# Kernel tuning notes

Hardware: AMD Instinct MI355X
Metric: run time of the kernel (lower is better)

Reference implementation:

```python
import jax, jax.numpy as jnp
import numpy as np

SQRT2 = 1.4142135623730951
B, C, T, J = 32, 4, 262144, 8


def _dw_corr(x, f):
    # depthwise VALID cross-correlation of (B,C,T) with 1-D filter f
    ch = x.shape[1]
    w = jnp.tile(f[None, None, :], (ch, 1, 1))  # (C,1,m)
    return jax.lax.conv_general_dilated(
        x, w, (1,), 'VALID', feature_group_count=ch,
        dimension_numbers=('NCH', 'OIH', 'NCH'))


def colfilter(x, h):
    # 'same' true convolution with odd-length filter h, zero padding
    p = h.shape[0] // 2
    xp = jnp.pad(x, ((0, 0), (0, 0), (p, p)))
    return _dw_corr(xp, jnp.flip(h))


def colifilt(x, ha, hb):
    # dtcwt synthesis upsampling filter bank (even-length qshift filters,
    # m//2 odd for 10-tap), zero extension (padding_mode='zeros').
    # Output length 2T; phase convention of dtcwt colifilt with ta=t, tb=t-1.
    b, c, t = x.shape
    m2 = ha.shape[0] // 2  # 5 for 10-tap qshift
    xp = jnp.pad(x, ((0, 0), (0, 0), (m2, m2)))  # length t+10
    L = t // 2 + 4
    seq_b = xp[:, :, 1::2][:, :, :L]      # padded indices 1,3,...,t+7
    seq_a = xp[:, :, 0::2][:, :, 1:L + 1]  # padded indices 2,4,...,t+8
    hao, hae = jnp.flip(ha[0::2]), jnp.flip(ha[1::2])  # odd/even taps of tree-a filter
    hbo, hbe = jnp.flip(hb[0::2]), jnp.flip(hb[1::2])
    y0 = _dw_corr(seq_b, hao)  # output samples 4s
    y1 = _dw_corr(seq_a, hbo)  # 4s+1
    y2 = _dw_corr(seq_b, hae)  # 4s+2
    y3 = _dw_corr(seq_a, hbe)  # 4s+3
    return jnp.stack([y0, y1, y2, y3], axis=-1).reshape(b, c, 2 * t)


def c2q(bp_r, bp_i, scale):
    # complex -> real: real part to even samples, imag part to odd samples
    b, c, th = bp_r.shape
    return (jnp.stack([bp_r, bp_i], axis=-1) * scale).reshape(b, c, 2 * th)


def inv_j2plus(lo, bp_r, bp_i, g0a, g1a, g0b, g1b):
    # one coarse synthesis level: interleave complex bandpass, then
    hi = c2q(bp_r, bp_i, SQRT2)
    return colifilt(lo, g0b, g0a) + colifilt(hi, g1b, g1a)


def inv_j1(lo, bp_r, bp_i, g0o, g1o):
    # finest synthesis level: full-rate biorthogonal filters, no upsampling
    hi = c2q(bp_r, bp_i, SQRT2)
    return colfilter(lo, g0o) + colfilter(hi, g1o)


def setup_inputs():
    key = jax.random.key(0)
    ks = jax.random.split(key, 32)
    inp = {}
    inp['yl'] = jax.random.normal(ks[0], (B, C, T // 2 ** (J - 1)), jnp.float32)
    for j in range(J):
        tj = T // 2 ** (j + 1)
        inp[f'yh{j}_r'] = jax.random.normal(ks[2 * j + 1], (B, C, tj), jnp.float32)
        inp[f'yh{j}_i'] = jax.random.normal(ks[2 * j + 2], (B, C, tj), jnp.float32)

    def filt(k, n):
        f = jax.random.normal(k, (n,), jnp.float32)
        return f / jnp.linalg.norm(f)

    inp['g0o'] = filt(ks[20], 7)   # near_sym_a synthesis lowpass (7-tap)
    inp['g1o'] = filt(ks[21], 5)   # near_sym_a synthesis highpass (5-tap)
    g0a = filt(ks[22], 10)         # qshift_a 10-tap
    g1a = filt(ks[23], 10)
    inp['g0a'], inp['g0b'] = g0a, jnp.flip(g0a)  # tree-b = time-reversed tree-a
    inp['g1a'], inp['g1b'] = g1a, jnp.flip(g1a)
    return inp


def reference(yl, yh0_r, yh0_i, yh1_r, yh1_i, yh2_r, yh2_i, yh3_r, yh3_i,
              yh4_r, yh4_i, yh5_r, yh5_i, yh6_r, yh6_i, yh7_r, yh7_i,
              g0o, g1o, g0a, g0b, g1a, g1b):
    yh = [(yh0_r, yh0_i), (yh1_r, yh1_i), (yh2_r, yh2_i), (yh3_r, yh3_i),
          (yh4_r, yh4_i), (yh5_r, yh5_i), (yh6_r, yh6_i), (yh7_r, yh7_i)]
    x = yl
    for j in range(J - 1, 0, -1):  # coarse-to-fine, doubles length each level
        x = inv_j2plus(x, yh[j][0], yh[j][1], g0a, g1a, g0b, g1b)
    return inv_j1(x, yh[0][0], yh[0][1], g0o, g1o)
```

## Files before the change

### kernel.cpp

```cpp
#include <hip/hip_runtime.h>

#define BLOCK 256
#define FT 1024

static __device__ __forceinline__ float ldz(const float* __restrict__ p, int i, int n) {
    return (i >= 0 && i < n) ? p[i] : 0.f;
}

struct QFilt {
    float b0e[5], b0o[5], a0e[5], a0o[5];
    float b1e[5], b1o[5], a1e[5], a1o[5];
};

static __device__ __forceinline__ QFilt load_qfilt(
    const float* __restrict__ g0a, const float* __restrict__ g0b,
    const float* __restrict__ g1a, const float* __restrict__ g1b) {
    const float S2 = 1.4142135623730951f;
    QFilt f;
#pragma unroll
    for (int i = 0; i < 5; ++i) {
        f.b0e[i] = g0b[8 - 2 * i]; f.b0o[i] = g0b[9 - 2 * i];
        f.a0e[i] = g0a[8 - 2 * i]; f.a0o[i] = g0a[9 - 2 * i];
        f.b1e[i] = S2 * g1b[8 - 2 * i]; f.b1o[i] = S2 * g1b[9 - 2 * i];
        f.a1e[i] = S2 * g1a[8 - 2 * i]; f.a1o[i] = S2 * g1a[9 - 2 * i];
    }
    return f;
}

static __device__ __forceinline__ float4 quad_i(
    const float* __restrict__ lo_s, int lobase,
    const float* __restrict__ r_s, const float* __restrict__ i_s, int ribase,
    const QFilt& f) {
    float y0 = 0.f, y1 = 0.f, y2 = 0.f, y3 = 0.f;
#pragma unroll
    for (int i = 0; i < 5; ++i) {
        float ve = lo_s[lobase + 2 * i], vo = lo_s[lobase + 2 * i + 1];
        float vr = r_s[ribase + i], vi = i_s[ribase + i];
        y0 = fmaf(ve, f.b0e[i], y0); y2 = fmaf(ve, f.b0o[i], y2);
        y1 = fmaf(vo, f.a0e[i], y1); y3 = fmaf(vo, f.a0o[i], y3);
        y0 = fmaf(vr, f.b1e[i], y0); y2 = fmaf(vr, f.b1o[i], y2);
        y1 = fmaf(vi, f.a1e[i], y1); y3 = fmaf(vi, f.a1o[i], y3);
    }
    return make_float4(y0, y1, y2, y3);
}

static __device__ __forceinline__ float4 quad_d(
    const float* __restrict__ Ae, const float* __restrict__ Ao, int base,
    const float* __restrict__ r_s, const float* __restrict__ i_s, int ribase,
    const QFilt& f) {
    float y0 = 0.f, y1 = 0.f, y2 = 0.f, y3 = 0.f;
#pragma unroll
    for (int i = 0; i < 5; ++i) {
        float ve = Ae[base + i], vo = Ao[base + i];
        float vr = r_s[ribase + i], vi = i_s[ribase + i];
        y0 = fmaf(ve, f.b0e[i], y0); y2 = fmaf(ve, f.b0o[i], y2);
        y1 = fmaf(vo, f.a0e[i], y1); y3 = fmaf(vo, f.a0o[i], y3);
        y0 = fmaf(vr, f.b1e[i], y0); y2 = fmaf(vr, f.b1o[i], y2);
        y1 = fmaf(vi, f.a1e[i], y1); y3 = fmaf(vi, f.a1o[i], y3);
    }
    return make_float4(y0, y1, y2, y3);
}

__global__ void __launch_bounds__(BLOCK) pair_lvl(
    const float* __restrict__ up,
    const float* __restrict__ ru, const float* __restrict__ iu,
    const float* __restrict__ rl, const float* __restrict__ il,
    float* __restrict__ out,
    const float* __restrict__ g0a, const float* __restrict__ g0b,
    const float* __restrict__ g1a, const float* __restrict__ g1b,
    int L)
{
    __shared__ __align__(16) float upw[272], ruw[140], iuw[140], rlw[264], ilw[264];
    __shared__ __align__(16) float Ae[260], Ao[260];
    int tid = threadIdx.x, bx = blockIdx.x, row = blockIdx.y;
    int lup = L >> 2, lu8 = L >> 3, lql = L >> 2;
    const float* uprow = up + (size_t)row * lup;
    const float* rurow = ru + (size_t)row * lu8;
    const float* iurow = iu + (size_t)row * lu8;
    const float* rlrow = rl + (size_t)row * lql;
    const float* ilrow = il + (size_t)row * lql;
    bool bnd = (bx == 0) || (bx == (int)gridDim.x - 1);
    int S = bx << 8;
    int sAu = (S >> 1) - 1;
    int gu = S - 8;
    int gru = (S >> 1) - 4;
    int grl = S - 4;

    for (int i = tid; i < 270; i += BLOCK) {
        const float* src; float* dst; int k, gb, len;
        if (i < 68)       { src = uprow; dst = upw; k = i;       gb = gu + 4 * k;  len = lup; }
        else if (i < 103) { src = rurow; dst = ruw; k = i - 68;  gb = gru + 4 * k; len = lu8; }
        else if (i < 138) { src = iurow; dst = iuw; k = i - 103; gb = gru + 4 * k; len = lu8; }
        else if (i < 204) { src = rlrow; dst = rlw; k = i - 138; gb = grl + 4 * k; len = lql; }
        else              { src = ilrow; dst = ilw; k = i - 204; gb = grl + 4 * k; len = lql; }
        float4 v;
        if (!bnd) v = *reinterpret_cast<const float4*>(src + gb);
        else { v.x = ldz(src, gb, len); v.y = ldz(src, gb + 1, len);
               v.z = ldz(src, gb + 2, len); v.w = ldz(src, gb + 3, len); }
        *reinterpret_cast<float4*>(dst + 4 * k) = v;
    }
    __syncthreads();

    QFilt f = load_qfilt(g0a, g0b, g1a, g1b);
    if (tid < 130) {
        float4 q = quad_i(upw, 2 * tid + 2, ruw, iuw, tid + 1, f);
        if (bnd) {
            int sp = sAu + tid;
            if (sp < 0 || sp >= lu8) q = make_float4(0.f, 0.f, 0.f, 0.f);
        }
        Ae[2 * tid] = q.x; Ae[2 * tid + 1] = q.z;
        Ao[2 * tid] = q.y; Ao[2 * tid + 1] = q.w;
    }
    __syncthreads();

    float4 res = quad_d(Ae, Ao, tid, rlw, ilw, tid + 2, f);
    reinterpret_cast<float4*>(out + (size_t)row * L)[S + tid] = res;
}

__global__ void __launch_bounds__(BLOCK) final4_lvl(
    const float* __restrict__ x4,
    const float* __restrict__ r3, const float* __restrict__ i3,
    const float* __restrict__ r2, const float* __restrict__ i2,
    const float* __restrict__ r1, const float* __restrict__ i1,
    const float* __restrict__ r0, const float* __restrict__ i0,
    float* __restrict__ out,
    const float* __restrict__ g0a, const float* __restrict__ g0b,
    const float* __restrict__ g1a, const float* __restrict__ g1b,
    const float* __restrict__ g0o, const float* __restrict__ g1o,
    int T_)
{
    const float S2 = 1.4142135623730951f;
    __shared__ __align__(16) float x4w[152], r3w[80], i3w[80];
    __shared__ __align__(16) float r2w[144], i2w[144];
    __shared__ __align__(16) float r1w[264], i1w[264];
    __shared__ __align__(16) float x3s[280], x2s[528];
    __shared__ __align__(16) float4 x1q[258];

    int row = blockIdx.y, tid = threadIdx.x;
    int n0 = blockIdx.x * FT;
    int t2 = T_ >> 1, t4 = T_ >> 2, t8 = T_ >> 3, t16 = T_ >> 4;
    int s0 = n0 >> 2, u0 = n0 >> 3, v0 = n0 >> 4, h0 = n0 >> 1;
    const float* x4row = x4 + (size_t)row * t8;
    const float* r3row = r3 + (size_t)row * t16;
    const float* i3row = i3 + (size_t)row * t16;
    const float* r2row = r2 + (size_t)row * t8;
    const float* i2row = i2 + (size_t)row * t8;
    const float* r1row = r1 + (size_t)row * t4;
    const float* i1row = i1 + (size_t)row * t4;
    const float* r0row = r0 + (size_t)row * t2;
    const float* i0row = i0 + (size_t)row * t2;
    bool bnd = (blockIdx.x == 0) || ((int)blockIdx.x == (int)gridDim.x - 1);

    float rA[4], iA[4];
    {
        int u0e = h0 + 2 * tid - 1;
        if (!bnd) {
            float4 va = *reinterpret_cast<const float4*>(r0row + u0e);
            float4 vb = *reinterpret_cast<const float4*>(i0row + u0e);
            rA[0] = va.x; rA[1] = va.y; rA[2] = va.z; rA[3] = va.w;
            iA[0] = vb.x; iA[1] = vb.y; iA[2] = vb.z; iA[3] = vb.w;
        } else {
#pragma unroll
            for (int e = 0; e < 4; ++e) {
                rA[e] = ldz(r0row, u0e + e, t2);
                iA[e] = ldz(i0row, u0e + e, t2);
            }
        }
    }
    float g0r[7], g1r[5];
#pragma unroll
    for (int j = 0; j < 7; ++j) g0r[j] = g0o[j];
#pragma unroll
    for (int j = 0; j < 5; ++j) g1r[j] = S2 * g1o[j];

    for (int i = tid; i < 277; i += BLOCK) {
        const float* src; float* dst; int k, gb, len;
        if (i < 37)       { src = x4row; dst = x4w; k = i;       gb = 2 * v0 - 8 + 4 * k; len = t8; }
        else if (i < 56)  { src = r3row; dst = r3w; k = i - 37;  gb = v0 - 4 + 4 * k;     len = t16; }
        else if (i < 75)  { src = i3row; dst = i3w; k = i - 56;  gb = v0 - 4 + 4 * k;     len = t16; }
        else if (i < 110) { src = r2row; dst = r2w; k = i - 75;  gb = u0 - 4 + 4 * k;     len = t8; }
        else if (i < 145) { src = i2row; dst = i2w; k = i - 110; gb = u0 - 4 + 4 * k;     len = t8; }
        else if (i < 211) { src = r1row; dst = r1w; k = i - 145; gb = s0 - 4 + 4 * k;     len = t4; }
        else              { src = i1row; dst = i1w; k = i - 211; gb = s0 - 4 + 4 * k;     len = t4; }
        float4 v;
        if (!bnd) v = *reinterpret_cast<const float4*>(src + gb);
        else { v.x = ldz(src, gb, len); v.y = ldz(src, gb + 1, len);
               v.z = ldz(src, gb + 2, len); v.w = ldz(src, gb + 3, len); }
        *reinterpret_cast<float4*>(dst + 4 * k) = v;
    }
    __syncthreads();

    QFilt f = load_qfilt(g0a, g0b, g1a, g1b);

    if (tid < 69) {
        int k = tid;
        float4 q = quad_i(x4w, 2 * k, r3w, i3w, k, f);
        if (bnd) {
            int v = v0 - 2 + k;
            if (v < 0 || v >= t16) q = make_float4(0.f, 0.f, 0.f, 0.f);
        }
        reinterpret_cast<float4*>(x3s)[k] = q;
    }
    __syncthreads();

    if (tid < 132) {
        int k = tid;
        float4 q = quad_i(x3s, 2 * k, r2w, i2w, k, f);
        if (bnd) {
            int u = u0 - 2 + k;
            if (u < 0 || u >= t8) q = make_float4(0.f, 0.f, 0.f, 0.f);
        }
        reinterpret_cast<float4*>(x2s)[k] = q;
    }
    __syncthreads();

    float4 myq;
    {
        int l = tid;
        float4 q = quad_i(x2s, 2 * l + 2, r1w, i1w, l + 1, f);
        if (bnd) {
            int s = s0 - 1 + l;
            if (s < 0 || s >= t4) q = make_float4(0.f, 0.f, 0.f, 0.f);
        }
        myq = q;
        x1q[l] = q;
        if (tid < 2) {
            int l2 = 256 + tid;
            q = quad_i(x2s, 2 * l2 + 2, r1w, i1w, l2 + 1, f);
            if (bnd) {
                int s = s0 - 1 + l2;
                if (s < 0 || s >= t4) q = make_float4(0.f, 0.f, 0.f, 0.f);
            }
            x1q[l2] = q;
        }
    }
    __syncthreads();

    float w[12];
    *reinterpret_cast<float4*>(&w[0]) = myq;
    *reinterpret_cast<float4*>(&w[4]) = x1q[tid + 1];
    *reinterpret_cast<float4*>(&w[8]) = x1q[tid + 2];

    float o[4];
#pragma unroll
    for (int p = 0; p < 4; ++p) {
        float acc = 0.f;
#pragma unroll
        for (int j = 0; j < 7; ++j)
            acc = fmaf(g0r[j], w[p + 7 - j], acc);
#pragma unroll
        for (int j = 0; j < 5; ++j) {
            int e = p + 4 - j;
            float v = (e & 1) ? iA[e >> 1] : rA[e >> 1];
            acc = fmaf(g1r[j], v, acc);
        }
        o[p] = acc;
    }
    reinterpret_cast<float4*>(out + (size_t)row * T_)[s0 + tid] =
        make_float4(o[0], o[1], o[2], o[3]);
}

extern "C" void kernel_launch(void* const* d_in, const int* in_sizes, int n_in,
                              void* d_out, int out_size, void* d_ws, size_t ws_size,
                              hipStream_t stream)
{
    const float* yl = (const float*)d_in[0];
    const float* yhr[8]; const float* yhi[8];
    for (int j = 0; j < 8; ++j) {
        yhr[j] = (const float*)d_in[1 + 2 * j];
        yhi[j] = (const float*)d_in[2 + 2 * j];
    }
    const float* g0o = (const float*)d_in[17];
    const float* g1o = (const float*)d_in[18];
    const float* g0a = (const float*)d_in[19];
    const float* g0b = (const float*)d_in[20];
    const float* g1a = (const float*)d_in[21];
    const float* g1b = (const float*)d_in[22];

    const int BC = 32 * 4;
    const int T_ = 262144;

    float* x4buf = (float*)d_ws;
    float* x6buf = (float*)((char*)d_ws + ((size_t)32 << 20));

    {
        dim3 grid(8192 / 1024, BC);
        pair_lvl<<<grid, BLOCK, 0, stream>>>(
            yl, yhr[7], yhi[7], yhr[6], yhi[6], x6buf,
            g0a, g0b, g1a, g1b, 8192);
    }
    {
        dim3 grid(32768 / 1024, BC);
        pair_lvl<<<grid, BLOCK, 0, stream>>>(
            x6buf, yhr[5], yhi[5], yhr[4], yhi[4], x4buf,
            g0a, g0b, g1a, g1b, 32768);
    }
    dim3 grid(T_ / FT, BC);
    final4_lvl<<<grid, BLOCK, 0, stream>>>(
        x4buf, yhr[3], yhi[3], yhr[2], yhi[2], yhr[1], yhi[1],
        yhr[0], yhi[0], (float*)d_out,
        g0a, g0b, g1a, g1b, g0o, g1o, T_);
}
```

Baseline: 127.6 us.

## Make final four-level kernel persistent with register-prefetched next-tile loads

Converts the final synthesis kernel into a persistent grid of 32 blocks per row. Each block loops over tiles with a stride and prefetches the next tile's inputs into registers while it computes the current one, overlapping global loads with the LDS filter stages. It also swaps __syncthreads for an explicit lgkmcnt wait plus s_barrier, so barriers do not wait on outstanding global prefetches. Filter loads and setup are hoisted out of the tile loop. The cost is a much smaller grid (4096 blocks instead of 32768), which may leave the GPU with less parallelism to hide latency, and more live registers from the prefetch buffers.

Measured after the change: 144.2 us. +13.0%, slower.

```diff
diff --git a/kernel.cpp b/kernel.cpp
--- a/kernel.cpp
+++ b/kernel.cpp
@@ -2,6 +2,12 @@
 
 #define BLOCK 256
 #define FT 1024
+#define PSTRIDE 32
+
+#define BAR_LGKM() do { \
+    asm volatile("s_waitcnt lgkmcnt(0)" ::: "memory"); \
+    __builtin_amdgcn_s_barrier(); \
+} while (0)
 
 static __device__ __forceinline__ float ldz(const float* __restrict__ p, int i, int n) {
     return (i >= 0 && i < n) ? p[i] : 0.f;
@@ -117,7 +123,7 @@
     reinterpret_cast<float4*>(out + (size_t)row * L)[S + tid] = res;
 }
 
-__global__ void __launch_bounds__(BLOCK) final4_lvl(
+__global__ void __launch_bounds__(BLOCK) final4_persist(
     const float* __restrict__ x4,
     const float* __restrict__ r3, const float* __restrict__ i3,
     const float* __restrict__ r2, const float* __restrict__ i2,
@@ -137,9 +143,8 @@
     __shared__ __align__(16) float4 x1q[258];
 
     int row = blockIdx.y, tid = threadIdx.x;
-    int n0 = blockIdx.x * FT;
     int t2 = T_ >> 1, t4 = T_ >> 2, t8 = T_ >> 3, t16 = T_ >> 4;
-    int s0 = n0 >> 2, u0 = n0 >> 3, v0 = n0 >> 4, h0 = n0 >> 1;
+    int NT = T_ >> 10;
     const float* x4row = x4 + (size_t)row * t8;
     const float* r3row = r3 + (size_t)row * t16;
     const float* i3row = i3 + (size_t)row * t16;
@@ -149,115 +154,167 @@
     const float* i1row = i1 + (size_t)row * t4;
     const float* r0row = r0 + (size_t)row * t2;
     const float* i0row = i0 + (size_t)row * t2;
-    bool bnd = (blockIdx.x == 0) || ((int)blockIdx.x == (int)gridDim.x - 1);
-
-    float rA[4], iA[4];
-    {
-        int u0e = h0 + 2 * tid - 1;
-        if (!bnd) {
-            float4 va = *reinterpret_cast<const float4*>(r0row + u0e);
-            float4 vb = *reinterpret_cast<const float4*>(i0row + u0e);
-            rA[0] = va.x; rA[1] = va.y; rA[2] = va.z; rA[3] = va.w;
-            iA[0] = vb.x; iA[1] = vb.y; iA[2] = vb.z; iA[3] = vb.w;
+
+    const float* src0; float* dst0; int A0, C0, len0;
+    {
+        int i = tid, k;
+        if (i < 37)       { src0 = x4row; k = i;       dst0 = x4w + 4 * k; A0 = 128; C0 = -8 + 4 * k; len0 = t8; }
+        else if (i < 56)  { src0 = r3row; k = i - 37;  dst0 = r3w + 4 * k; A0 = 64;  C0 = -4 + 4 * k; len0 = t16; }
+        else if (i < 75)  { src0 = i3row; k = i - 56;  dst0 = i3w + 4 * k; A0 = 64;  C0 = -4 + 4 * k; len0 = t16; }
+        else if (i < 110) { src0 = r2row; k = i - 75;  dst0 = r2w + 4 * k; A0 = 128; C0 = -4 + 4 * k; len0 = t8; }
+        else if (i < 145) { src0 = i2row; k = i - 110; dst0 = i2w + 4 * k; A0 = 128; C0 = -4 + 4 * k; len0 = t8; }
+        else if (i < 211) { src0 = r1row; k = i - 145; dst0 = r1w + 4 * k; A0 = 256; C0 = -4 + 4 * k; len0 = t4; }
+        else              { src0 = i1row; k = i - 211; dst0 = i1w + 4 * k; A0 = 256; C0 = -4 + 4 * k; len0 = t4; }
+    }
+    bool has1 = (tid < 21);
+    int k1 = tid + 45;
+    float* dst1 = i1w + 4 * k1;
+    int C1 = -4 + 4 * k1;
+
+    QFilt f = load_qfilt(g0a, g0b, g1a, g1b);
+    float g0r[7], g1r[5];
+#pragma unroll
+    for (int j = 0; j < 7; ++j) g0r[j] = g0o[j];
+#pragma unroll
+    for (int j = 0; j < 5; ++j) g1r[j] = S2 * g1o[j];
+
+    int tile = blockIdx.x;
+    bool bndc = (tile == 0) || (tile == NT - 1);
+    float4 pv0, pv1 = make_float4(0.f, 0.f, 0.f, 0.f);
+    {
+        int gb = A0 * tile + C0;
+        if (!bndc) pv0 = *reinterpret_cast<const float4*>(src0 + gb);
+        else { pv0.x = ldz(src0, gb, len0); pv0.y = ldz(src0, gb + 1, len0);
+               pv0.z = ldz(src0, gb + 2, len0); pv0.w = ldz(src0, gb + 3, len0); }
+        if (has1) {
+            int gb1 = 256 * tile + C1;
+            if (!bndc) pv1 = *reinterpret_cast<const float4*>(i1row + gb1);
+            else { pv1.x = ldz(i1row, gb1, t4); pv1.y = ldz(i1row, gb1 + 1, t4);
+                   pv1.z = ldz(i1row, gb1 + 2, t4); pv1.w = ldz(i1row, gb1 + 3, t4); }
+        }
+    }
+    float4 prA_c, piA_c, prA_n = make_float4(0,0,0,0), piA_n = make_float4(0,0,0,0);
+    {
+        int u0e = (tile << 9) + 2 * tid - 1;
+        if (!bndc) {
+            prA_c = *reinterpret_cast<const float4*>(r0row + u0e);
+            piA_c = *reinterpret_cast<const float4*>(i0row + u0e);
         } else {
-#pragma unroll
-            for (int e = 0; e < 4; ++e) {
-                rA[e] = ldz(r0row, u0e + e, t2);
-                iA[e] = ldz(i0row, u0e + e, t2);
-            }
-        }
-    }
-    float g0r[7], g1r[5];
-#pragma unroll
-    for (int j = 0; j < 7; ++j) g0r[j] = g0o[j];
-#pragma unroll
-    for (int j = 0; j < 5; ++j) g1r[j] = S2 * g1o[j];
-
-    for (int i = tid; i < 277; i += BLOCK) {
-        const float* src; float* dst; int k, gb, len;
-        if (i < 37)       { src = x4row; dst = x4w; k = i;       gb = 2 * v0 - 8 + 4 * k; len = t8; }
-        else if (i < 56)  { src = r3row; dst = r3w; k = i - 37;  gb = v0 - 4 + 4 * k;     len = t16; }
-        else if (i < 75)  { src = i3row; dst = i3w; k = i - 56;  gb = v0 - 4 + 4 * k;     len = t16; }
-        else if (i < 110) { src = r2row; dst = r2w; k = i - 75;  gb = u0 - 4 + 4 * k;     len = t8; }
-        else if (i < 145) { src = i2row; dst = i2w; k = i - 110; gb = u0 - 4 + 4 * k;     len = t8; }
-        else if (i < 211) { src = r1row; dst = r1w; k = i - 145; gb = s0 - 4 + 4 * k;     len = t4; }
-        else              { src = i1row; dst = i1w; k = i - 211; gb = s0 - 4 + 4 * k;     len = t4; }
-        float4 v;
-        if (!bnd) v = *reinterpret_cast<const float4*>(src + gb);
-        else { v.x = ldz(src, gb, len); v.y = ldz(src, gb + 1, len);
-               v.z = ldz(src, gb + 2, len); v.w = ldz(src, gb + 3, len); }
-        *reinterpret_cast<float4*>(dst + 4 * k) = v;
-    }
-    __syncthreads();
-
-    QFilt f = load_qfilt(g0a, g0b, g1a, g1b);
-
-    if (tid < 69) {
-        int k = tid;
-        float4 q = quad_i(x4w, 2 * k, r3w, i3w, k, f);
-        if (bnd) {
-            int v = v0 - 2 + k;
-            if (v < 0 || v >= t16) q = make_float4(0.f, 0.f, 0.f, 0.f);
-        }
-        reinterpret_cast<float4*>(x3s)[k] = q;
-    }
-    __syncthreads();
-
-    if (tid < 132) {
-        int k = tid;
-        float4 q = quad_i(x3s, 2 * k, r2w, i2w, k, f);
-        if (bnd) {
-            int u = u0 - 2 + k;
-            if (u < 0 || u >= t8) q = make_float4(0.f, 0.f, 0.f, 0.f);
-        }
-        reinterpret_cast<float4*>(x2s)[k] = q;
-    }
-    __syncthreads();
-
-    float4 myq;
-    {
-        int l = tid;
-        float4 q = quad_i(x2s, 2 * l + 2, r1w, i1w, l + 1, f);
-        if (bnd) {
-            int s = s0 - 1 + l;
-            if (s < 0 || s >= t4) q = make_float4(0.f, 0.f, 0.f, 0.f);
-        }
-        myq = q;
-        x1q[l] = q;
-        if (tid < 2) {
-            int l2 = 256 + tid;
-            q = quad_i(x2s, 2 * l2 + 2, r1w, i1w, l2 + 1, f);
-            if (bnd) {
-                int s = s0 - 1 + l2;
+            prA_c.x = ldz(r0row, u0e, t2);     prA_c.y = ldz(r0row, u0e + 1, t2);
+            prA_c.z = ldz(r0row, u0e + 2, t2); prA_c.w = ldz(r0row, u0e + 3, t2);
+            piA_c.x = ldz(i0row, u0e, t2);     piA_c.y = ldz(i0row, u0e + 1, t2);
+            piA_c.z = ldz(i0row, u0e + 2, t2); piA_c.w = ldz(i0row, u0e + 3, t2);
+        }
+    }
+
+    bool bndn = false;
+    while (true) {
+        *reinterpret_cast<float4*>(dst0) = pv0;
+        if (has1) *reinterpret_cast<float4*>(dst1) = pv1;
+        BAR_LGKM();
+
+        int ntile = tile + PSTRIDE;
+        bool nvalid = ntile < NT;
+        if (nvalid) {
+            bndn = (ntile == NT - 1);
+            int gb = A0 * ntile + C0;
+            if (!bndn) pv0 = *reinterpret_cast<const float4*>(src0 + gb);
+            else { pv0.x = ldz(src0, gb, len0); pv0.y = ldz(src0, gb + 1, len0);
+                   pv0.z = ldz(src0, gb + 2, len0); pv0.w = ldz(src0, gb + 3, len0); }
+            if (has1) {
+                int gb1 = 256 * ntile + C1;
+                if (!bndn) pv1 = *reinterpret_cast<const float4*>(i1row + gb1);
+                else { pv1.x = ldz(i1row, gb1, t4); pv1.y = ldz(i1row, gb1 + 1, t4);
+                       pv1.z = ldz(i1row, gb1 + 2, t4); pv1.w = ldz(i1row, gb1 + 3, t4); }
+            }
+            int u0e = (ntile << 9) + 2 * tid - 1;
+            if (!bndn) {
+                prA_n = *reinterpret_cast<const float4*>(r0row + u0e);
+                piA_n = *reinterpret_cast<const float4*>(i0row + u0e);
+            } else {
+                prA_n.x = ldz(r0row, u0e, t2);     prA_n.y = ldz(r0row, u0e + 1, t2);
+                prA_n.z = ldz(r0row, u0e + 2, t2); prA_n.w = ldz(r0row, u0e + 3, t2);
+                piA_n.x = ldz(i0row, u0e, t2);     piA_n.y = ldz(i0row, u0e + 1, t2);
+                piA_n.z = ldz(i0row, u0e + 2, t2); piA_n.w = ldz(i0row, u0e + 3, t2);
+            }
+        }
+
+        int s0 = tile << 8, u0 = tile << 7, v0 = tile << 6;
+
+        if (tid < 69) {
+            int k = tid;
+            float4 q = quad_i(x4w, 2 * k, r3w, i3w, k, f);
+            if (bndc) {
+                int v = v0 - 2 + k;
+                if (v < 0 || v >= t16) q = make_float4(0.f, 0.f, 0.f, 0.f);
+            }
+            reinterpret_cast<float4*>(x3s)[k] = q;
+        }
+        BAR_LGKM();
+
+        if (tid < 132) {
+            int k = tid;
+            float4 q = quad_i(x3s, 2 * k, r2w, i2w, k, f);
+            if (bndc) {
+                int u = u0 - 2 + k;
+                if (u < 0 || u >= t8) q = make_float4(0.f, 0.f, 0.f, 0.f);
+            }
+            reinterpret_cast<float4*>(x2s)[k] = q;
+        }
+        BAR_LGKM();
+
+        float4 myq;
+        {
+            int l = tid;
+            float4 q = quad_i(x2s, 2 * l + 2, r1w, i1w, l + 1, f);
+            if (bndc) {
+                int s = s0 - 1 + l;
                 if (s < 0 || s >= t4) q = make_float4(0.f, 0.f, 0.f, 0.f);
             }
-            x1q[l2] = q;
-        }
-    }
-    __syncthreads();
-
-    float w[12];
-    *reinterpret_cast<float4*>(&w[0]) = myq;
-    *reinterpret_cast<float4*>(&w[4]) = x1q[tid + 1];
-    *reinterpret_cast<float4*>(&w[8]) = x1q[tid + 2];
-
-    float o[4];
-#pragma unroll
-    for (int p = 0; p < 4; ++p) {
-        float acc = 0.f;
-#pragma unroll
-        for (int j = 0; j < 7; ++j)
-            acc = fmaf(g0r[j], w[p + 7 - j], acc);
-#pragma unroll
-        for (int j = 0; j < 5; ++j) {
-            int e = p + 4 - j;
-            float v = (e & 1) ? iA[e >> 1] : rA[e >> 1];
-            acc = fmaf(g1r[j], v, acc);
-        }
-        o[p] = acc;
-    }
-    reinterpret_cast<float4*>(out + (size_t)row * T_)[s0 + tid] =
-        make_float4(o[0], o[1], o[2], o[3]);
+            myq = q;
+            x1q[l] = q;
+            if (tid < 2) {
+                int l2 = 256 + tid;
+                q = quad_i(x2s, 2 * l2 + 2, r1w, i1w, l2 + 1, f);
+                if (bndc) {
+                    int s = s0 - 1 + l2;
+                    if (s < 0 || s >= t4) q = make_float4(0.f, 0.f, 0.f, 0.f);
+                }
+                x1q[l2] = q;
+            }
+        }
+        BAR_LGKM();
+
+        float w[12];
+        *reinterpret_cast<float4*>(&w[0]) = myq;
+        *reinterpret_cast<float4*>(&w[4]) = x1q[tid + 1];
+        *reinterpret_cast<float4*>(&w[8]) = x1q[tid + 2];
+
+        float rAv[4] = { prA_c.x, prA_c.y, prA_c.z, prA_c.w };
+        float iAv[4] = { piA_c.x, piA_c.y, piA_c.z, piA_c.w };
+
+        float o[4];
+#pragma unroll
+        for (int p = 0; p < 4; ++p) {
+            float acc = 0.f;
+#pragma unroll
+            for (int j = 0; j < 7; ++j)
+                acc = fmaf(g0r[j], w[p + 7 - j], acc);
+#pragma unroll
+            for (int j = 0; j < 5; ++j) {
+                int e = p + 4 - j;
+                float v = (e & 1) ? iAv[e >> 1] : rAv[e >> 1];
+                acc = fmaf(g1r[j], v, acc);
+            }
+            o[p] = acc;
+        }
+        reinterpret_cast<float4*>(out + (size_t)row * T_)[s0 + tid] =
+            make_float4(o[0], o[1], o[2], o[3]);
+
+        if (!nvalid) break;
+        tile = ntile; bndc = bndn;
+        prA_c = prA_n; piA_c = piA_n;
+    }
 }
 
 extern "C" void kernel_launch(void* const* d_in, const int* in_sizes, int n_in,
@@ -295,8 +352,8 @@
             x6buf, yhr[5], yhi[5], yhr[4], yhi[4], x4buf,
             g0a, g0b, g1a, g1b, 32768);
     }
-    dim3 grid(T_ / FT, BC);
-    final4_lvl<<<grid, BLOCK, 0, stream>>>(
+    dim3 grid(PSTRIDE, BC);
+    final4_persist<<<grid, BLOCK, 0, stream>>>(
         x4buf, yhr[3], yhi[3], yhr[2], yhi[2], yhr[1], yhi[1],
         yhr[0], yhi[0], (float*)d_out,
         g0a, g0b, g1a, g1b, g0o, g1o, T_);
```

## Make final four-level synthesis wave-independent with per-wave tiles and no barriers

Applied to the files above, without the earlier changes.

The final fused kernel now gives each 64-lane wave its own 256-sample output tile and private shared-memory region, replacing block-wide __syncthreads with an LDS waitcnt between stages. This removes block barriers and lets waves progress independently. The cost is a larger halo per output sample: each wave recomputes its own overlap at levels 3, 2 and 1, so loads and redundant compute go up. It also relies on wave-lockstep LDS visibility, which is only safe because each wave touches just its own region.

New measurement: 145.6 us. 14.1% more time.

```diff
diff --git a/kernel.cpp b/kernel.cpp
--- a/kernel.cpp
+++ b/kernel.cpp
@@ -1,11 +1,12 @@
 #include <hip/hip_runtime.h>
 
 #define BLOCK 256
-#define FT 1024
 
 static __device__ __forceinline__ float ldz(const float* __restrict__ p, int i, int n) {
     return (i >= 0 && i < n) ? p[i] : 0.f;
 }
+
+#define WAVE_SYNC() asm volatile("s_waitcnt lgkmcnt(0)" ::: "memory")
 
 struct QFilt {
     float b0e[5], b0o[5], a0e[5], a0o[5];
@@ -25,6 +26,22 @@
         f.a1e[i] = S2 * g1a[8 - 2 * i]; f.a1o[i] = S2 * g1a[9 - 2 * i];
     }
     return f;
+}
+
+static __device__ __forceinline__ float4 quad_w(
+    const float* base, int loOff, int riOff, int ioff, const QFilt& f) {
+    float y0 = 0.f, y1 = 0.f, y2 = 0.f, y3 = 0.f;
+#pragma unroll
+    for (int i = 0; i < 5; ++i) {
+        float2 lo2 = *reinterpret_cast<const float2*>(base + loOff + 2 * i);
+        float ve = lo2.x, vo = lo2.y;
+        float vr = base[riOff + i], vi = base[riOff + ioff + i];
+        y0 = fmaf(ve, f.b0e[i], y0); y2 = fmaf(ve, f.b0o[i], y2);
+        y1 = fmaf(vo, f.a0e[i], y1); y3 = fmaf(vo, f.a0o[i], y3);
+        y0 = fmaf(vr, f.b1e[i], y0); y2 = fmaf(vr, f.b1o[i], y2);
+        y1 = fmaf(vi, f.a1e[i], y1); y3 = fmaf(vi, f.a1o[i], y3);
+    }
+    return make_float4(y0, y1, y2, y3);
 }
 
 static __device__ __forceinline__ float4 quad_i(
@@ -117,7 +134,19 @@
     reinterpret_cast<float4*>(out + (size_t)row * L)[S + tid] = res;
 }
 
-__global__ void __launch_bounds__(BLOCK) final4_lvl(
+#define O_X4 0
+#define O_R3 48
+#define O_I3 72
+#define O_R2 96
+#define O_I2 136
+#define O_R1 176
+#define O_I1 248
+#define O_X3 320
+#define O_X2 400
+#define O_X1 544
+#define WSTR 816
+
+__global__ void __launch_bounds__(BLOCK) final4_wave(
     const float* __restrict__ x4,
     const float* __restrict__ r3, const float* __restrict__ i3,
     const float* __restrict__ r2, const float* __restrict__ i2,
@@ -130,16 +159,18 @@
     int T_)
 {
     const float S2 = 1.4142135623730951f;
-    __shared__ __align__(16) float x4w[152], r3w[80], i3w[80];
-    __shared__ __align__(16) float r2w[144], i2w[144];
-    __shared__ __align__(16) float r1w[264], i1w[264];
-    __shared__ __align__(16) float x3s[280], x2s[528];
-    __shared__ __align__(16) float4 x1q[258];
-
-    int row = blockIdx.y, tid = threadIdx.x;
-    int n0 = blockIdx.x * FT;
+    __shared__ __align__(16) float S[4 * WSTR];
+
+    int tid = threadIdx.x;
+    int lane = tid & 63, wv = tid >> 6;
+    int row = blockIdx.y;
     int t2 = T_ >> 1, t4 = T_ >> 2, t8 = T_ >> 3, t16 = T_ >> 4;
-    int s0 = n0 >> 2, u0 = n0 >> 3, v0 = n0 >> 4, h0 = n0 >> 1;
+    int NT256 = T_ >> 8;
+    int widx = blockIdx.x * 4 + wv;
+    int n0 = widx << 8;
+    int s0 = widx << 6, u0 = widx << 5, v0 = widx << 4, h0 = widx << 7;
+    float* W = S + wv * WSTR;
+
     const float* x4row = x4 + (size_t)row * t8;
     const float* r3row = r3 + (size_t)row * t16;
     const float* i3row = i3 + (size_t)row * t16;
@@ -149,11 +180,11 @@
     const float* i1row = i1 + (size_t)row * t4;
     const float* r0row = r0 + (size_t)row * t2;
     const float* i0row = i0 + (size_t)row * t2;
-    bool bnd = (blockIdx.x == 0) || ((int)blockIdx.x == (int)gridDim.x - 1);
+    bool bnd = (widx == 0) || (widx == NT256 - 1);
 
     float rA[4], iA[4];
     {
-        int u0e = h0 + 2 * tid - 1;
+        int u0e = h0 + 2 * lane - 1;
         if (!bnd) {
             float4 va = *reinterpret_cast<const float4*>(r0row + u0e);
             float4 vb = *reinterpret_cast<const float4*>(i0row + u0e);
@@ -167,79 +198,85 @@
             }
         }
     }
+
+    {
+#pragma unroll
+        for (int s = 0; s < 2; ++s) {
+            int i = lane + 64 * s;
+            if (s == 1 && lane >= 16) break;
+            const float* src; int k, gb, len, doff;
+            if (i < 12)      { src = x4row; k = i;      gb = 2*v0 - 8 + 4*k; len = t8;  doff = O_X4 + 4*k; }
+            else if (i < 18) { src = r3row; k = i - 12; gb = v0 - 4 + 4*k;   len = t16; doff = O_R3 + 4*k; }
+            else if (i < 24) { src = i3row; k = i - 18; gb = v0 - 4 + 4*k;   len = t16; doff = O_I3 + 4*k; }
+            else if (i < 34) { src = r2row; k = i - 24; gb = u0 - 4 + 4*k;   len = t8;  doff = O_R2 + 4*k; }
+            else if (i < 44) { src = i2row; k = i - 34; gb = u0 - 4 + 4*k;   len = t8;  doff = O_I2 + 4*k; }
+            else if (i < 62) { src = r1row; k = i - 44; gb = s0 - 4 + 4*k;   len = t4;  doff = O_R1 + 4*k; }
+            else             { src = i1row; k = i - 62; gb = s0 - 4 + 4*k;   len = t4;  doff = O_I1 + 4*k; }
+            float4 v;
+            if (!bnd) v = *reinterpret_cast<const float4*>(src + gb);
+            else { v.x = ldz(src, gb, len); v.y = ldz(src, gb + 1, len);
+                   v.z = ldz(src, gb + 2, len); v.w = ldz(src, gb + 3, len); }
+            *reinterpret_cast<float4*>(W + doff) = v;
+        }
+    }
+
+    QFilt f = load_qfilt(g0a, g0b, g1a, g1b);
     float g0r[7], g1r[5];
 #pragma unroll
     for (int j = 0; j < 7; ++j) g0r[j] = g0o[j];
 #pragma unroll
     for (int j = 0; j < 5; ++j) g1r[j] = S2 * g1o[j];
 
-    for (int i = tid; i < 277; i += BLOCK) {
-        const float* src; float* dst; int k, gb, len;
-        if (i < 37)       { src = x4row; dst = x4w; k = i;       gb = 2 * v0 - 8 + 4 * k; len = t8; }
-        else if (i < 56)  { src = r3row; dst = r3w; k = i - 37;  gb = v0 - 4 + 4 * k;     len = t16; }
-        else if (i < 75)  { src = i3row; dst = i3w; k = i - 56;  gb = v0 - 4 + 4 * k;     len = t16; }
-        else if (i < 110) { src = r2row; dst = r2w; k = i - 75;  gb = u0 - 4 + 4 * k;     len = t8; }
-        else if (i < 145) { src = i2row; dst = i2w; k = i - 110; gb = u0 - 4 + 4 * k;     len = t8; }
-        else if (i < 211) { src = r1row; dst = r1w; k = i - 145; gb = s0 - 4 + 4 * k;     len = t4; }
-        else              { src = i1row; dst = i1w; k = i - 211; gb = s0 - 4 + 4 * k;     len = t4; }
-        float4 v;
-        if (!bnd) v = *reinterpret_cast<const float4*>(src + gb);
-        else { v.x = ldz(src, gb, len); v.y = ldz(src, gb + 1, len);
-               v.z = ldz(src, gb + 2, len); v.w = ldz(src, gb + 3, len); }
-        *reinterpret_cast<float4*>(dst + 4 * k) = v;
-    }
-    __syncthreads();
-
-    QFilt f = load_qfilt(g0a, g0b, g1a, g1b);
-
-    if (tid < 69) {
-        int k = tid;
-        float4 q = quad_i(x4w, 2 * k, r3w, i3w, k, f);
+    WAVE_SYNC();
+
+    if (lane < 20) {
+        int k = lane;
+        float4 q = quad_w(W, O_X4 + 2 * k, O_R3 + k, 24, f);
         if (bnd) {
             int v = v0 - 2 + k;
             if (v < 0 || v >= t16) q = make_float4(0.f, 0.f, 0.f, 0.f);
         }
-        reinterpret_cast<float4*>(x3s)[k] = q;
-    }
-    __syncthreads();
-
-    if (tid < 132) {
-        int k = tid;
-        float4 q = quad_i(x3s, 2 * k, r2w, i2w, k, f);
+        *reinterpret_cast<float4*>(W + O_X3 + 4 * k) = q;
+    }
+    WAVE_SYNC();
+
+    if (lane < 36) {
+        int k = lane;
+        float4 q = quad_w(W, O_X3 + 2 * k, O_R2 + k, 40, f);
         if (bnd) {
             int u = u0 - 2 + k;
             if (u < 0 || u >= t8) q = make_float4(0.f, 0.f, 0.f, 0.f);
         }
-        reinterpret_cast<float4*>(x2s)[k] = q;
-    }
-    __syncthreads();
+        *reinterpret_cast<float4*>(W + O_X2 + 4 * k) = q;
+    }
+    WAVE_SYNC();
 
     float4 myq;
     {
-        int l = tid;
-        float4 q = quad_i(x2s, 2 * l + 2, r1w, i1w, l + 1, f);
+        int l = lane;
+        float4 q = quad_w(W, O_X2 + 2 * l + 2, O_R1 + l + 1, 72, f);
         if (bnd) {
             int s = s0 - 1 + l;
             if (s < 0 || s >= t4) q = make_float4(0.f, 0.f, 0.f, 0.f);
         }
         myq = q;
-        x1q[l] = q;
-        if (tid < 2) {
-            int l2 = 256 + tid;
-            q = quad_i(x2s, 2 * l2 + 2, r1w, i1w, l2 + 1, f);
+        *reinterpret_cast<float4*>(W + O_X1 + 4 * l) = q;
+        if (lane < 2) {
+            int l2 = 64 + lane;
+            q = quad_w(W, O_X2 + 2 * l2 + 2, O_R1 + l2 + 1, 72, f);
             if (bnd) {
                 int s = s0 - 1 + l2;
                 if (s < 0 || s >= t4) q = make_float4(0.f, 0.f, 0.f, 0.f);
             }
-            x1q[l2] = q;
-        }
-    }
-    __syncthreads();
+            *reinterpret_cast<float4*>(W + O_X1 + 4 * l2) = q;
+        }
+    }
+    WAVE_SYNC();
 
     float w[12];
     *reinterpret_cast<float4*>(&w[0]) = myq;
-    *reinterpret_cast<float4*>(&w[4]) = x1q[tid + 1];
-    *reinterpret_cast<float4*>(&w[8]) = x1q[tid + 2];
+    *reinterpret_cast<float4*>(&w[4]) = *reinterpret_cast<float4*>(W + O_X1 + 4 * (lane + 1));
+    *reinterpret_cast<float4*>(&w[8]) = *reinterpret_cast<float4*>(W + O_X1 + 4 * (lane + 2));
 
     float o[4];
 #pragma unroll
@@ -256,7 +293,7 @@
         }
         o[p] = acc;
     }
-    reinterpret_cast<float4*>(out + (size_t)row * T_)[s0 + tid] =
+    reinterpret_cast<float4*>(out + (size_t)row * T_)[s0 + lane] =
         make_float4(o[0], o[1], o[2], o[3]);
 }
 
@@ -295,8 +332,8 @@
             x6buf, yhr[5], yhi[5], yhr[4], yhi[4], x4buf,
             g0a, g0b, g1a, g1b, 32768);
     }
-    dim3 grid(T_ / FT, BC);
-    final4_lvl<<<grid, BLOCK, 0, stream>>>(
+    dim3 grid((T_ >> 8) / 4, BC);
+    final4_wave<<<grid, BLOCK, 0, stream>>>(
         x4buf, yhr[3], yhi[3], yhr[2], yhi[2], yhr[1], yhi[1],
         yhr[0], yhi[0], (float*)d_out,
         g0a, g0b, g1a, g1b, g0o, g1o, T_);
```
